# Kernel tuning notes

Measured on AMD Instinct MI355X. Metric: run time of the kernel, lower is better.

Reference implementation:

```python
import jax, jax.numpy as jnp
import numpy as np

EMB_DIM = 128
NUM_CLS = 128
H = W = 512
K = 131072


def setup_inputs() -> dict:
    key = jax.random.key(0)
    k1, k2, k3, k4 = jax.random.split(key, 4)
    gc_features = jax.random.normal(k1, (1, EMB_DIM, H, W), dtype=jnp.float32)
    cls_id_map = jax.random.randint(k2, (1, K), 0, H * W, dtype=jnp.int64)
    # nn.Linear(emb_dim, num_cls) params, kaiming-uniform-ish scale
    lim = 1.0 / np.sqrt(EMB_DIM)
    W_cls = jax.random.uniform(k3, (NUM_CLS, EMB_DIM), dtype=jnp.float32, minval=-lim, maxval=lim)
    b_cls = jax.random.uniform(k4, (NUM_CLS,), dtype=jnp.float32, minval=-lim, maxval=lim)
    return {"gc_features": gc_features, "cls_id_map": cls_id_map, "W_cls": W_cls, "b_cls": b_cls}


def reference(gc_features, cls_id_map, W_cls, b_cls):
    B, C, h, w = gc_features.shape
    # _tranpose_and_gather_feat: [B,C,H,W] -> [B,HW,C], gather rows by inds
    feat = gc_features.reshape(B, C, h * w).transpose(0, 2, 1)      # [B, HW, C]
    feat = jnp.take_along_axis(feat, cls_id_map[:, :, None], axis=1)  # [B, K, C]
    feat = feat[0]                                                   # squeeze(0) -> [K, C]
    pred = feat @ W_cls.T + b_cls                                    # [K, num_cls]
    return jax.nn.softmax(pred, axis=1)
```

## Files before the change

### kernel.cpp

```cpp
#include <hip/hip_runtime.h>
#include <hip/hip_bf16.h>

#define HW      262144
#define NCH     128
#define NCLS    128
#define KROWS   131072
#define BM      64
#define LDK     136

typedef short  bf16x8 __attribute__((ext_vector_type(8)));
typedef float  f32x4  __attribute__((ext_vector_type(4)));

__device__ inline ushort f2bf(float f) {
    union { float f; unsigned u; } v; v.f = f;
    unsigned u = v.u;
    unsigned r = (u + 0x7FFFu + ((u >> 16) & 1u)) >> 16;
    return (ushort)r;
}

__device__ inline float bf2f(ushort b) {
    union { unsigned u; float f; } v; v.u = ((unsigned)b) << 16;
    return v.f;
}

__global__ __launch_bounds__(256) void gemm_logits(const float* __restrict__ gc,
                                                   const float* __restrict__ Wc,
                                                   ushort* __restrict__ pred) {
    __shared__ ushort Wl[NCLS * LDK];
    __shared__ ushort Al[BM   * LDK];

    const int t    = threadIdx.x;
    const int lane = t & 63;
    const int wv   = t >> 6;
    const int tx   = t & 63;
    const int ty   = t >> 6;

    for (int i = 0; i < 64; ++i) {
        int e = (i << 8) + t;
        int n = e >> 7, c = e & 127;
        Wl[n * LDK + c] = f2bf(Wc[e]);
    }

    const int l15   = lane & 15;
    const int khalf = (lane >> 4) << 3;
    const int mrow  = (wv << 4) + l15;
    const int rbase = (lane >> 4) << 2;

    for (int tile = 0; tile < 2; ++tile) {
        const int m0 = (blockIdx.x * 2 + tile) * BM;

        __syncthreads();

        #pragma unroll
        for (int cc = 0; cc < 16; ++cc) {
            int c0 = (ty << 5) + (cc << 1);
            float v0 = gc[(size_t)c0 * HW + m0 + tx];
            float v1 = gc[(size_t)(c0 + 1) * HW + m0 + tx];
            ushort2 pk; pk.x = f2bf(v0); pk.y = f2bf(v1);
            *(ushort2*)&Al[tx * LDK + c0] = pk;
        }
        __syncthreads();

        f32x4 acc[8];
        #pragma unroll
        for (int i = 0; i < 8; ++i) acc[i] = (f32x4){0.f, 0.f, 0.f, 0.f};

        #pragma unroll
        for (int kk = 0; kk < 4; ++kk) {
            const int ko = (kk << 5) + khalf;
            bf16x8 a = *(const bf16x8*)&Al[mrow * LDK + ko];
            #pragma unroll
            for (int nt = 0; nt < 8; ++nt) {
                bf16x8 b = *(const bf16x8*)&Wl[((nt << 4) + l15) * LDK + ko];
                acc[nt] = __builtin_amdgcn_mfma_f32_16x16x32_bf16(a, b, acc[nt], 0, 0, 0);
            }
        }

        #pragma unroll
        for (int nt = 0; nt < 8; ++nt) {
            #pragma unroll
            for (int r = 0; r < 4; ++r) {
                int row = m0 + (wv << 4) + rbase + r;
                int col = (nt << 4) + l15;
                pred[(size_t)row * NCLS + col] = f2bf(acc[nt][r]);
            }
        }
    }
}

__global__ __launch_bounds__(256) void gather_softmax(const ushort* __restrict__ pred,
                                                      const int* __restrict__ idx,
                                                      const float* __restrict__ bias,
                                                      float* __restrict__ out) {
    const int t    = threadIdx.x;
    const int lane = t & 63;
    const int wv   = t >> 6;

    const float2 bv = *(const float2*)&bias[lane << 1];
    const int kbase = (blockIdx.x << 3) + (wv << 1);

    #pragma unroll
    for (int r = 0; r < 2; ++r) {
        const int k = kbase + r;
        const int p = idx[k];
        const ushort2 lv = *(const ushort2*)&pred[(size_t)p * NCLS + (lane << 1)];
        float l0 = bf2f(lv.x) + bv.x;
        float l1 = bf2f(lv.y) + bv.y;
        float e0 = __expf(l0);
        float e1 = __expf(l1);
        float s = e0 + e1;
        #pragma unroll
        for (int m = 32; m; m >>= 1) s += __shfl_xor(s, m, 64);
        float inv = 1.0f / s;
        float2 o; o.x = e0 * inv; o.y = e1 * inv;
        *(float2*)&out[(size_t)k * NCLS + (lane << 1)] = o;
    }
}

extern "C" void kernel_launch(void* const* d_in, const int* in_sizes, int n_in,
                              void* d_out, int out_size, void* d_ws, size_t ws_size,
                              hipStream_t stream) {
    const float* gc   = (const float*)d_in[0];
    const int*   idx  = (const int*)d_in[1];
    const float* Wc   = (const float*)d_in[2];
    const float* bias = (const float*)d_in[3];
    float* out  = (float*)d_out;
    ushort* pred = (ushort*)d_ws;

    gemm_logits<<<dim3(HW / (2 * BM)), dim3(256), 0, stream>>>(gc, Wc, pred);
    gather_softmax<<<dim3(KROWS / 8), dim3(256), 0, stream>>>(pred, idx, bias, out);
}
```

Before: 265.5 us.

## Fuse bias and softmax into GEMM epilogue, store fp16 probs, pre-swizzle weights

Moves bias add and softmax into the dense GEMM over all HW pixels, which now writes fp16 probabilities through an LDS-staged coalesced store. The gather kernel becomes a plain fp16-to-fp32 row copy. A new small kernel converts W to bf16 in MFMA fragment order, using the output buffer as scratch, and the GEMM loads it into LDS with global_load_lds. A-tile loads now use float4 into a fragment-ordered LDS layout. The trade-off is running softmax over 262144 rows instead of 131072 gathered ones, and fp16 probabilities lose some precision.

```diff
diff --git a/kernel.cpp b/kernel.cpp
--- a/kernel.cpp
+++ b/kernel.cpp
@@ -1,12 +1,13 @@
 #include <hip/hip_runtime.h>
 #include <hip/hip_bf16.h>
+#include <hip/hip_fp16.h>
 
 #define HW      262144
 #define NCH     128
 #define NCLS    128
 #define KROWS   131072
 #define BM      64
-#define LDK     136
+#define OLP     144
 
 typedef short  bf16x8 __attribute__((ext_vector_type(8)));
 typedef float  f32x4  __attribute__((ext_vector_type(4)));
@@ -18,33 +19,43 @@
     return (ushort)r;
 }
 
-__device__ inline float bf2f(ushort b) {
-    union { unsigned u; float f; } v; v.u = ((unsigned)b) << 16;
-    return v.f;
+__global__ __launch_bounds__(256) void wconv(const float* __restrict__ Wc,
+                                             ushort* __restrict__ Wf) {
+    int e    = blockIdx.x * 256 + threadIdx.x;
+    int j    = e & 7;
+    int slot = e >> 3;
+    int lane = slot & 63;
+    int kk   = (slot >> 6) & 3;
+    int nt   = slot >> 8;
+    int n = (nt << 4) + (lane & 15);
+    int k = (kk << 5) + ((lane >> 4) << 3) + j;
+    Wf[e] = f2bf(Wc[n * NCH + k]);
 }
 
-__global__ __launch_bounds__(256) void gemm_logits(const float* __restrict__ gc,
-                                                   const float* __restrict__ Wc,
-                                                   ushort* __restrict__ pred) {
-    __shared__ ushort Wl[NCLS * LDK];
-    __shared__ ushort Al[BM   * LDK];
+__global__ __launch_bounds__(256) void gemm_probs(const float* __restrict__ gc,
+                                                  const ushort* __restrict__ Wf,
+                                                  const float* __restrict__ bias,
+                                                  ushort* __restrict__ pred) {
+    __shared__ ushort Wl[NCLS * NCH];
+    __shared__ ushort AO[BM * OLP];
 
     const int t    = threadIdx.x;
     const int lane = t & 63;
     const int wv   = t >> 6;
-    const int tx   = t & 63;
-    const int ty   = t >> 6;
+    const int l15  = lane & 15;
 
-    for (int i = 0; i < 64; ++i) {
-        int e = (i << 8) + t;
-        int n = e >> 7, c = e & 127;
-        Wl[n * LDK + c] = f2bf(Wc[e]);
+    #pragma unroll
+    for (int i = 0; i < 8; ++i) {
+        const ushort* g = Wf + (i << 11) + (t << 3);
+        ushort*       l = Wl + (i << 11) + (t << 3);
+        __builtin_amdgcn_global_load_lds(
+            (const __attribute__((address_space(1))) unsigned*)g,
+            (__attribute__((address_space(3))) unsigned*)l, 16, 0, 0);
     }
 
-    const int l15   = lane & 15;
-    const int khalf = (lane >> 4) << 3;
-    const int mrow  = (wv << 4) + l15;
-    const int rbase = (lane >> 4) << 2;
+    float bcol[8];
+    #pragma unroll
+    for (int nt = 0; nt < 8; ++nt) bcol[nt] = bias[(nt << 4) + l15];
 
     for (int tile = 0; tile < 2; ++tile) {
         const int m0 = (blockIdx.x * 2 + tile) * BM;
@@ -52,12 +63,28 @@
         __syncthreads();
 
         #pragma unroll
-        for (int cc = 0; cc < 16; ++cc) {
-            int c0 = (ty << 5) + (cc << 1);
-            float v0 = gc[(size_t)c0 * HW + m0 + tx];
-            float v1 = gc[(size_t)(c0 + 1) * HW + m0 + tx];
-            ushort2 pk; pk.x = f2bf(v0); pk.y = f2bf(v1);
-            *(ushort2*)&Al[tx * LDK + c0] = pk;
+        for (int i = 0; i < 4; ++i) {
+            int q  = (i << 8) + t;
+            int cp = q >> 4;
+            int mq = q & 15;
+            int c0 = cp << 1;
+            int m  = mq << 2;
+            float4 v0 = *(const float4*)&gc[(size_t)c0 * HW + m0 + m];
+            float4 v1 = *(const float4*)&gc[(size_t)(c0 + 1) * HW + m0 + m];
+            int kk = c0 >> 5;
+            int hi = ((c0 >> 3) & 3) << 4;
+            int j  = c0 & 7;
+            const float* a0 = (const float*)&v0;
+            const float* a1 = (const float*)&v1;
+            #pragma unroll
+            for (int d = 0; d < 4; ++d) {
+                int row   = m + d;
+                int lslot = (row & 15) + hi;
+                int mt    = row >> 4;
+                int addr  = ((((mt << 2) + kk) << 6) + lslot) << 3;
+                __hip_bfloat162 pk = __float22bfloat162_rn(make_float2(a0[d], a1[d]));
+                *(ushort2*)&AO[addr + j] = *(ushort2*)&pk;
+            }
         }
         __syncthreads();
 
@@ -67,53 +94,71 @@
 
         #pragma unroll
         for (int kk = 0; kk < 4; ++kk) {
-            const int ko = (kk << 5) + khalf;
-            bf16x8 a = *(const bf16x8*)&Al[mrow * LDK + ko];
+            bf16x8 a = *(const bf16x8*)&AO[((((wv << 2) + kk) << 6) + lane) << 3];
             #pragma unroll
             for (int nt = 0; nt < 8; ++nt) {
-                bf16x8 b = *(const bf16x8*)&Wl[((nt << 4) + l15) * LDK + ko];
+                bf16x8 b = *(const bf16x8*)&Wl[((((nt << 2) + kk) << 6) + lane) << 3];
                 acc[nt] = __builtin_amdgcn_mfma_f32_16x16x32_bf16(a, b, acc[nt], 0, 0, 0);
             }
         }
 
+        float pr[8][4];
         #pragma unroll
-        for (int nt = 0; nt < 8; ++nt) {
+        for (int rr = 0; rr < 4; ++rr) {
+            float ex[8], s = 0.f;
             #pragma unroll
-            for (int r = 0; r < 4; ++r) {
-                int row = m0 + (wv << 4) + rbase + r;
-                int col = (nt << 4) + l15;
-                pred[(size_t)row * NCLS + col] = f2bf(acc[nt][r]);
+            for (int nt = 0; nt < 8; ++nt) {
+                ex[nt] = __expf(acc[nt][rr] + bcol[nt]);
+                s += ex[nt];
             }
+            s += __shfl_xor(s, 1, 64);
+            s += __shfl_xor(s, 2, 64);
+            s += __shfl_xor(s, 4, 64);
+            s += __shfl_xor(s, 8, 64);
+            float inv = 1.0f / s;
+            #pragma unroll
+            for (int nt = 0; nt < 8; ++nt) pr[nt][rr] = ex[nt] * inv;
+        }
+
+        __syncthreads();
+
+        const int rowb = (wv << 4) + ((lane >> 4) << 2);
+        #pragma unroll
+        for (int nt = 0; nt < 8; ++nt)
+            #pragma unroll
+            for (int rr = 0; rr < 4; ++rr)
+                AO[(rowb + rr) * OLP + (nt << 4) + l15] =
+                    __half_as_ushort(__float2half_rn(pr[nt][rr]));
+        __syncthreads();
+
+        #pragma unroll
+        for (int i = 0; i < 4; ++i) {
+            int q   = (i << 8) + t;
+            int row = q >> 4;
+            int ch  = q & 15;
+            int4 v = *(const int4*)&AO[row * OLP + (ch << 3)];
+            *(int4*)&pred[(size_t)(m0 + row) * NCLS + (ch << 3)] = v;
         }
     }
 }
 
-__global__ __launch_bounds__(256) void gather_softmax(const ushort* __restrict__ pred,
-                                                      const int* __restrict__ idx,
-                                                      const float* __restrict__ bias,
-                                                      float* __restrict__ out) {
+__global__ __launch_bounds__(256) void gather_rows(const ushort* __restrict__ pred,
+                                                   const int* __restrict__ idx,
+                                                   float* __restrict__ out) {
     const int t    = threadIdx.x;
     const int lane = t & 63;
     const int wv   = t >> 6;
+    const int kbase = (blockIdx.x << 4) + (wv << 2);
 
-    const float2 bv = *(const float2*)&bias[lane << 1];
-    const int kbase = (blockIdx.x << 3) + (wv << 1);
+    int p[4];
+    #pragma unroll
+    for (int r = 0; r < 4; ++r) p[r] = idx[kbase + r];
 
     #pragma unroll
-    for (int r = 0; r < 2; ++r) {
-        const int k = kbase + r;
-        const int p = idx[k];
-        const ushort2 lv = *(const ushort2*)&pred[(size_t)p * NCLS + (lane << 1)];
-        float l0 = bf2f(lv.x) + bv.x;
-        float l1 = bf2f(lv.y) + bv.y;
-        float e0 = __expf(l0);
-        float e1 = __expf(l1);
-        float s = e0 + e1;
-        #pragma unroll
-        for (int m = 32; m; m >>= 1) s += __shfl_xor(s, m, 64);
-        float inv = 1.0f / s;
-        float2 o; o.x = e0 * inv; o.y = e1 * inv;
-        *(float2*)&out[(size_t)k * NCLS + (lane << 1)] = o;
+    for (int r = 0; r < 4; ++r) {
+        __half2 h = *(const __half2*)&pred[(size_t)p[r] * NCLS + (lane << 1)];
+        float2 f = __half22float2(h);
+        *(float2*)&out[(size_t)(kbase + r) * NCLS + (lane << 1)] = f;
     }
 }
 
@@ -124,9 +169,12 @@
     const int*   idx  = (const int*)d_in[1];
     const float* Wc   = (const float*)d_in[2];
     const float* bias = (const float*)d_in[3];
-    float* out  = (float*)d_out;
+    float*  out  = (float*)d_out;
     ushort* pred = (ushort*)d_ws;
 
-    gemm_logits<<<dim3(HW / (2 * BM)), dim3(256), 0, stream>>>(gc, Wc, pred);
-    gather_softmax<<<dim3(KROWS / 8), dim3(256), 0, stream>>>(pred, idx, bias, out);
+    ushort* Wf = (ushort*)d_out;
+
+    wconv<<<dim3(64), dim3(256), 0, stream>>>(Wc, Wf);
+    gemm_probs<<<dim3(HW / (2 * BM)), dim3(256), 0, stream>>>(gc, Wf, bias, pred);
+    gather_rows<<<dim3(KROWS / 16), dim3(256), 0, stream>>>(pred, idx, out);
 }
```

New measurement: 243.4 us. -8.3%, faster.
